# Optimization experiments

Hardware: AMD Instinct MI355X
Metric: run time of the kernel (lower is better)

The kernel has to match this reference:

```python
import jax, jax.numpy as jnp
import numpy as np

B, N, D, F_IN, E, RATIO, C, HEADS, KERNELS = 128, 512, 128, 128, 524288, 128, 10, 4, 3
ALPHA = 0.5


def setup_inputs() -> dict:
    key = jax.random.key(0)
    ks = jax.random.split(key, 20)

    def w(k, shape, fan):
        return (jax.random.normal(k, shape, jnp.float32) / np.float32(np.sqrt(fan)))

    gid = jnp.arange(E, dtype=jnp.int32) // (E // B)
    src = gid * N + jax.random.randint(ks[0], (E,), 0, N, dtype=jnp.int32)
    dst = gid * N + jax.random.randint(ks[1], (E,), 0, N, dtype=jnp.int32)
    edge_index = jnp.stack([src, dst]).astype(jnp.int32)
    return {
        'x': jax.random.normal(ks[2], (B * N, F_IN), jnp.float32),
        'edge_index': edge_index,
        'enc_w': w(ks[3], (F_IN, D), F_IN), 'enc_b': jnp.zeros((D,), jnp.float32),
        'gconv_w': w(ks[4], (3, KERNELS, D, D), D), 'gconv_b': jnp.zeros((3, KERNELS, D), jnp.float32),
        'wg1_w': w(ks[5], (D,), D), 'wg1_b': jnp.zeros((1,), jnp.float32),
        'wg2_w': w(ks[6], (D,), D), 'wg2_b': jnp.zeros((1,), jnp.float32),
        'pg1_w': w(ks[7], (D,), D), 'pg1_b': jnp.zeros((1,), jnp.float32),
        'pg2_w': w(ks[8], (D,), D), 'pg2_b': jnp.zeros((1,), jnp.float32),
        'q_w': w(ks[9], (D, D), D), 'q_b': jnp.zeros((D,), jnp.float32),
        'k_w': w(ks[10], (D, D), D), 'k_b': jnp.zeros((D,), jnp.float32),
        'v_w': w(ks[11], (D, D), D), 'v_b': jnp.zeros((D,), jnp.float32),
        'o_w': w(ks[12], (D, D), D), 'o_b': jnp.zeros((D,), jnp.float32),
        'ro_w': w(ks[13], (RATIO,), RATIO), 'ro_b': jnp.zeros((1,), jnp.float32),
        'c1_w': w(ks[14], (D, D), D), 'c1_b': jnp.zeros((D,), jnp.float32),
        'c2_w': w(ks[15], (D, C), D), 'c2_b': jnp.zeros((C,), jnp.float32),
    }


def _make_gcn(edge_index, n):
    # PyG GCNConv: add self-loops, symmetric normalization D^-1/2 (A+I) D^-1/2
    src, dst = edge_index[0], edge_index[1]
    deg = jax.ops.segment_sum(jnp.ones(src.shape[0], jnp.float32), dst, num_segments=n) + 1.0
    dinv = jax.lax.rsqrt(deg)
    norm = dinv[src] * dinv[dst]          # [E]
    self_norm = dinv * dinv               # self-loop coefficient

    def gcn(x, W, b):
        h = x @ W                                                  # [n, out]
        out = jax.ops.segment_sum(h[src] * norm[:, None], dst, num_segments=n)
        return out + h * self_norm[:, None] + b
    return gcn


def _forward(x, edge_index, enc_w, enc_b, gconv_w, gconv_b,
             wg1_w, wg1_b, wg2_w, wg2_b, pg1_w, pg1_b, pg2_w, pg2_b,
             q_w, q_b, k_w, k_b, v_w, v_b, o_w, o_b, ro_w, ro_b,
             c1_w, c1_b, c2_w, c2_b):
    n = x.shape[0]
    gcn = _make_gcn(edge_index, n)
    h = x @ enc_w + enc_b                   # node encoder (dropout: eval mode)

    def mkgc(hin, Ws, bs):                  # sum of relu(GCNConv) over kernels
        out = jax.nn.relu(gcn(hin, Ws[0], bs[0]))
        for kk in range(1, Ws.shape[0]):
            out = out + jax.nn.relu(gcn(hin, Ws[kk], bs[kk]))
        return out

    x1 = mkgc(h, gconv_w[0], gconv_b[0])
    x2 = mkgc(x1, gconv_w[1], gconv_b[1])
    x3 = mkgc(x2, gconv_w[2], gconv_b[2])

    def gla_score(xi, w1, b1, w2, b2):      # GLAPool(flag=1): global + local score
        s1 = xi @ w1[:, None] + b1          # [n,1]
        s2 = gcn(xi, w2[:, None], b2)       # [n,1]
        return ALPHA * s1 + (1.0 - ALPHA) * s2

    wts = jnp.concatenate([gla_score(xi, wg1_w, wg1_b, wg2_w, wg2_b)
                           for xi in (x1, x2, x3)], axis=-1)        # [n,3]
    wts = jax.nn.softmax(wts, axis=-1)
    xf = wts[:, 0:1] * x1 + wts[:, 1:2] * x2 + wts[:, 2:3] * x3

    # GLAPool top-k pooling (uniform graph sizes -> dense [B,N])
    score = gla_score(xf, pg1_w, pg1_b, pg2_w, pg2_b)[:, 0].reshape(B, N)
    vals, idx = jax.lax.top_k(score, RATIO)                          # [B,RATIO]
    xd = xf.reshape(B, N, D)
    xp = jnp.take_along_axis(xd, idx[:, :, None], axis=1) * jnp.tanh(vals)[:, :, None]

    # MAB: Q from pooled nodes, K/V = GCNConv over full graph
    dh = D // HEADS
    Qh = (xp @ q_w + q_b).reshape(B, RATIO, HEADS, dh)
    K = gcn(xf, k_w, k_b).reshape(B, N, HEADS, dh)
    V = gcn(xf, v_w, v_b).reshape(B, N, HEADS, dh)
    att = jnp.einsum('bqhd,bkhd->bhqk', Qh, K) / jnp.sqrt(jnp.float32(D))
    A = jax.nn.softmax(att, axis=-1)
    O = Qh + jnp.einsum('bhqk,bkhd->bqhd', A, V)
    O = O.reshape(B, RATIO, D)
    O = O + jax.nn.relu(O @ o_w + o_b)

    # Conv1d(ratio, 1, 1) readout == learned weighted sum over pooled slots
    xg = jnp.einsum('r,brd->bd', ro_w, O) + ro_b                     # [B,D]

    hc = jax.nn.relu(xg @ c1_w + c1_b)
    logp = jax.nn.log_softmax(hc @ c2_w + c2_b, axis=-1)
    return logp, xg


def reference(x, edge_index, enc_w, enc_b, gconv_w, gconv_b,
              wg1_w, wg1_b, wg2_w, wg2_b, pg1_w, pg1_b, pg2_w, pg2_b,
              q_w, q_b, k_w, k_b, v_w, v_b, o_w, o_b, ro_w, ro_b,
              c1_w, c1_b, c2_w, c2_b):
    return _forward(x, edge_index, enc_w, enc_b, gconv_w, gconv_b,
                    wg1_w, wg1_b, wg2_w, wg2_b, pg1_w, pg1_b, pg2_w, pg2_b,
                    q_w, q_b, k_w, k_b, v_w, v_b, o_w, o_b, ro_w, ro_b,
                    c1_w, c1_b, c2_w, c2_b)
```

## Files before the change

kernel.cpp:

```cpp
#include <hip/hip_runtime.h>
#include <math.h>

#define N_NODES 65536
#define NE      524288
#define DD      128
#define BGRAPH  128
#define NPG     512
#define RATIO_K 128
#define NHEAD   4
#define DHEAD   32

typedef short bf16x8 __attribute__((ext_vector_type(8)));
typedef float f32x4 __attribute__((ext_vector_type(4)));

union U8 { unsigned short u[8]; bf16x8 v; };

__device__ __forceinline__ unsigned short f2b(float f) {
  unsigned u = __float_as_uint(f);
  unsigned r = u + 0x7fffu + ((u >> 16) & 1u);
  return (unsigned short)(r >> 16);
}
__device__ __forceinline__ float b2f(unsigned short h) {
  return __uint_as_float(((unsigned)h) << 16);
}
__device__ __forceinline__ void split3(float v, unsigned short& h, unsigned short& m, unsigned short& l) {
  h = f2b(v);
  float vm = v - b2f(h);
  m = f2b(vm);
  l = f2b(vm - b2f(m));
}


__global__ void count_kernel(const int* __restrict__ dst, int* __restrict__ cnt) {
  int e = blockIdx.x * 256 + threadIdx.x;
  if (e < NE) atomicAdd(&cnt[dst[e]], 1);
}

__global__ void dinv_kernel(const int* __restrict__ cnt, float* __restrict__ dinv) {
  int i = blockIdx.x * 256 + threadIdx.x;
  if (i < N_NODES) dinv[i] = rsqrtf((float)cnt[i] + 1.0f);
}

__global__ __launch_bounds__(512) void scan_kernel2(const int* __restrict__ cnt, int* __restrict__ rp) {
  __shared__ int part[512];
  int g = blockIdx.x, t = threadIdx.x;
  int v = cnt[g * 512 + t];
  part[t] = v;
  __syncthreads();
  for (int off = 1; off < 512; off <<= 1) {
    int u = (t >= off) ? part[t - off] : 0;
    __syncthreads();
    part[t] += u;
    __syncthreads();
  }
  rp[g * 512 + t] = g * 4096 + part[t] - v;
  if (g == BGRAPH - 1 && t == 511) rp[N_NODES] = NE;
}

__global__ void scatter_kernel(const int* __restrict__ edge, const int* __restrict__ rp,
                               int* __restrict__ fill, const float* __restrict__ dinv,
                               int* __restrict__ col, float* __restrict__ wgt) {
  int e = blockIdx.x * 256 + threadIdx.x;
  if (e >= NE) return;
  int s = edge[e];
  int d = edge[NE + e];
  int p = rp[d] + atomicAdd(&fill[d], 1);
  col[p] = s;
  wgt[p] = dinv[s] * dinv[d];
}

struct WPtrs { const float* p[14]; };

__global__ void wprep_all(WPtrs wp, unsigned short* __restrict__ dstBase) {
  int mat = blockIdx.y;
  int idx = blockIdx.x * 256 + threadIdx.x;
  const float* __restrict__ W = wp.p[mat];
  unsigned short* __restrict__ dst = dstBase + (size_t)mat * 49152;
  int k = idx >> 7, n = idx & 127;
  float v = W[k * 128 + n];
  unsigned short h, m, l;
  split3(v, h, m, l);
  dst[n * 128 + k] = h;
  dst[16384 + n * 128 + k] = m;
  dst[32768 + n * 128 + k] = l;
}

#define WROW 40

template<int NW, bool RELU, bool RES, bool DUAL>
__global__ __launch_bounds__(256, 2) void mfma_gemm8(
    const float* __restrict__ A,
    const unsigned short* __restrict__ Wt,
    const float* __restrict__ bias, const float* __restrict__ bias2,
    const float* __restrict__ res,
    float* __restrict__ out, float* __restrict__ out2) {
  __shared__ unsigned short Wlds[NW * 3 * 64 * WROW];
  int tid = threadIdx.x;
  int wave = tid >> 6, lane = tid & 63;
  int c16 = lane & 15, kg = lane >> 4;
  int wrow = (wave >> 1) * 32;
  int wcol = (wave & 1) * 32;
  size_t row0 = (size_t)blockIdx.y * 64 + wrow;
  int n0 = blockIdx.x * 64;

  f32x4 acc[NW][2][2];
  #pragma unroll
  for (int m = 0; m < NW; ++m)
    #pragma unroll
    for (int mi = 0; mi < 2; ++mi)
      #pragma unroll
      for (int ni = 0; ni < 2; ++ni) acc[m][mi][ni] = (f32x4){0.f, 0.f, 0.f, 0.f};

  for (int ks = 0; ks < 4; ++ks) {
    if (ks) __syncthreads();
    #pragma unroll
    for (int i = 0; i < NW * 3; ++i) {
      int c = tid + i * 256;
      int u4 = c & 3;
      int n = (c >> 2) & 63;
      int mp = c >> 8;
      *(uint4*)&Wlds[(mp * 64 + n) * WROW + u4 * 8] =
          *(const uint4*)&Wt[(size_t)mp * 16384 + (n0 + n) * 128 + ks * 32 + u4 * 8];
    }
    __syncthreads();

    bf16x8 a[2][3];
    #pragma unroll
    for (int mi = 0; mi < 2; ++mi) {
      const float* ap = A + (row0 + mi * 16 + c16) * 128 + ks * 32 + kg * 8;
      float4 f0 = *(const float4*)ap;
      float4 f1 = *(const float4*)(ap + 4);
      float f[8] = {f0.x, f0.y, f0.z, f0.w, f1.x, f1.y, f1.z, f1.w};
      U8 hh, mm, ll;
      #pragma unroll
      for (int j = 0; j < 8; ++j) split3(f[j], hh.u[j], mm.u[j], ll.u[j]);
      a[mi][0] = hh.v; a[mi][1] = mm.v; a[mi][2] = ll.v;
    }

    #pragma unroll
    for (int mat = 0; mat < NW; ++mat) {
      #pragma unroll
      for (int ni = 0; ni < 2; ++ni) {
        int nrow = (wcol >> 4) + ni;
        int off = ((mat * 3) * 64 + nrow * 16 + c16) * WROW + kg * 8;
        bf16x8 bh = *(const bf16x8*)&Wlds[off];
        bf16x8 bm = *(const bf16x8*)&Wlds[off + 64 * WROW];
        bf16x8 bl = *(const bf16x8*)&Wlds[off + 128 * WROW];
        #pragma unroll
        for (int mi = 0; mi < 2; ++mi) {
          acc[mat][mi][ni] = __builtin_amdgcn_mfma_f32_16x16x32_bf16(a[mi][0], bh, acc[mat][mi][ni], 0, 0, 0);
          acc[mat][mi][ni] = __builtin_amdgcn_mfma_f32_16x16x32_bf16(a[mi][0], bm, acc[mat][mi][ni], 0, 0, 0);
          acc[mat][mi][ni] = __builtin_amdgcn_mfma_f32_16x16x32_bf16(a[mi][1], bh, acc[mat][mi][ni], 0, 0, 0);
          acc[mat][mi][ni] = __builtin_amdgcn_mfma_f32_16x16x32_bf16(a[mi][0], bl, acc[mat][mi][ni], 0, 0, 0);
          acc[mat][mi][ni] = __builtin_amdgcn_mfma_f32_16x16x32_bf16(a[mi][2], bh, acc[mat][mi][ni], 0, 0, 0);
          acc[mat][mi][ni] = __builtin_amdgcn_mfma_f32_16x16x32_bf16(a[mi][1], bm, acc[mat][mi][ni], 0, 0, 0);
        }
      }
    }
  }

  #pragma unroll
  for (int mi = 0; mi < 2; ++mi)
    #pragma unroll
    for (int ni = 0; ni < 2; ++ni) {
      int colg = n0 + wcol + ni * 16 + c16;
      #pragma unroll
      for (int r = 0; r < 4; ++r) {
        size_t o = (row0 + mi * 16 + kg * 4 + r) * 128 + colg;
        if (DUAL) {
          out[o]  = acc[0][mi][ni][r] + bias[colg];
          out2[o] = acc[NW - 1][mi][ni][r] + bias2[colg];
        } else if (NW == 3) {
          float g = fmaxf(acc[0][mi][ni][r] + bias[colg], 0.f)
                  + fmaxf(acc[1][mi][ni][r] + bias[128 + colg], 0.f)
                  + fmaxf(acc[2][mi][ni][r] + bias[256 + colg], 0.f);
          out[o] = g;
        } else {
          float g = acc[0][mi][ni][r] + bias[colg];
          if (RELU) g = fmaxf(g, 0.f);
          if (RES) g += res[o];
          out[o] = g;
        }
      }
    }
}

__global__ __launch_bounds__(256) void gemm_k128(
    const float* __restrict__ A, const float* __restrict__ W,
    const float* __restrict__ bias, const float* __restrict__ res,
    float* __restrict__ out, int M, int do_relu) {
  __shared__ float As[8][64];
  __shared__ float Ws[8][128];
  int tid = threadIdx.x;
  int tx = tid & 15;
  int ty = tid >> 4;
  int row0 = blockIdx.x * 64;
  if (row0 >= M) return;
  const float* Ab = A + (size_t)row0 * DD;

  float acc[4][8];
  #pragma unroll
  for (int i = 0; i < 4; ++i)
    #pragma unroll
    for (int j = 0; j < 8; ++j) acc[i][j] = 0.f;

  for (int k0 = 0; k0 < 128; k0 += 8) {
    {
      int e = tid * 2;
      int r = e >> 3, kk = e & 7;
      float2 av = *(const float2*)&Ab[r * DD + k0 + kk];
      As[kk][r] = av.x;
      As[kk + 1][r] = av.y;
    }
    {
      int kk = tid >> 5, c = (tid & 31) * 4;
      float4 wv = *(const float4*)&W[(k0 + kk) * DD + c];
      *(float4*)&Ws[kk][c] = wv;
    }
    __syncthreads();
    #pragma unroll
    for (int kk = 0; kk < 8; ++kk) {
      float4 a4 = *(const float4*)&As[kk][ty * 4];
      float4 b0 = *(const float4*)&Ws[kk][tx * 8];
      float4 b1 = *(const float4*)&Ws[kk][tx * 8 + 4];
      float av[4] = {a4.x, a4.y, a4.z, a4.w};
      float bv[8] = {b0.x, b0.y, b0.z, b0.w, b1.x, b1.y, b1.z, b1.w};
      #pragma unroll
      for (int i = 0; i < 4; ++i)
        #pragma unroll
        for (int j = 0; j < 8; ++j) acc[i][j] += av[i] * bv[j];
    }
    __syncthreads();
  }
  #pragma unroll
  for (int i = 0; i < 4; ++i) {
    int r = row0 + ty * 4 + i;
    size_t base = (size_t)r * DD + tx * 8;
    #pragma unroll
    for (int j = 0; j < 8; ++j) {
      float g = acc[i][j];
      if (bias) g += bias[tx * 8 + j];
      if (do_relu) g = fmaxf(g, 0.f);
      if (res) g += res[base + j];
      out[base + j] = g;
    }
  }
}

__global__ __launch_bounds__(256) void agg4_kernel(
    const float* __restrict__ H, const int* __restrict__ rp, const int* __restrict__ col,
    const float* __restrict__ wgt, const float* __restrict__ dinv,
    float* __restrict__ out) {
  int g = blockIdx.x * 256 + threadIdx.x;
  int node = g >> 5;
  int l = g & 31;
  const float4* H4 = (const float4*)H;
  float dv = dinv[node];
  float4 acc = H4[(size_t)node * 32 + l];
  float sn = dv * dv;
  acc.x *= sn; acc.y *= sn; acc.z *= sn; acc.w *= sn;
  int beg = rp[node], end = rp[node + 1];
  for (int j = beg; j < end; ++j) {
    float w = wgt[j];
    int c = col[j];
    float4 hv = H4[(size_t)c * 32 + l];
    acc.x += w * hv.x; acc.y += w * hv.y; acc.z += w * hv.z; acc.w += w * hv.w;
  }
  ((float4*)out)[(size_t)node * 32 + l] = acc;
}

__global__ __launch_bounds__(256) void dot2_kernel(
    const float* __restrict__ X, const float* __restrict__ w1, const float* __restrict__ w2,
    float* __restrict__ t1, float* __restrict__ t2) {
  int node = (blockIdx.x * 256 + threadIdx.x) >> 6;
  int lane = threadIdx.x & 63;
  if (node >= N_NODES) return;
  const float* xr = X + (size_t)node * DD;
  float a = xr[lane], b = xr[lane + 64];
  float s1 = a * w1[lane] + b * w1[lane + 64];
  float s2 = a * w2[lane] + b * w2[lane + 64];
  #pragma unroll
  for (int off = 32; off > 0; off >>= 1) {
    s1 += __shfl_down(s1, off);
    s2 += __shfl_down(s2, off);
  }
  if (lane == 0) { t1[node] = s1; t2[node] = s2; }
}

__global__ void score_kernel(const float* __restrict__ t1, const float* __restrict__ t2,
                             const int* __restrict__ rp, const int* __restrict__ col,
                             const float* __restrict__ wgt, const float* __restrict__ dinv,
                             const float* __restrict__ b1p, const float* __restrict__ b2p,
                             float* __restrict__ out) {
  int i = blockIdx.x * 256 + threadIdx.x;
  if (i >= N_NODES) return;
  float dv = dinv[i];
  float a2 = dv * dv * t2[i] + b2p[0];
  int beg = rp[i], end = rp[i + 1];
  for (int j = beg; j < end; ++j) a2 += wgt[j] * t2[col[j]];
  out[i] = 0.5f * (t1[i] + b1p[0]) + 0.5f * a2;
}

__global__ void xf_kernel(const float* __restrict__ x1, const float* __restrict__ x2,
                          const float* __restrict__ x3, const float* __restrict__ sc,
                          float* __restrict__ xf) {
  size_t idx = (size_t)blockIdx.x * 256 + threadIdx.x;
  int i = (int)(idx >> 5);
  float s0 = sc[i], s1 = sc[N_NODES + i], s2 = sc[2 * N_NODES + i];
  float mx = fmaxf(s0, fmaxf(s1, s2));
  float e0 = __expf(s0 - mx), e1 = __expf(s1 - mx), e2 = __expf(s2 - mx);
  float inv = 1.f / (e0 + e1 + e2);
  e0 *= inv; e1 *= inv; e2 *= inv;
  float4 a = ((const float4*)x1)[idx];
  float4 b = ((const float4*)x2)[idx];
  float4 c = ((const float4*)x3)[idx];
  float4 o;
  o.x = e0 * a.x + e1 * b.x + e2 * c.x;
  o.y = e0 * a.y + e1 * b.y + e2 * c.y;
  o.z = e0 * a.z + e1 * b.z + e2 * c.z;
  o.w = e0 * a.w + e1 * b.w + e2 * c.w;
  ((float4*)xf)[idx] = o;
}

__global__ __launch_bounds__(512) void topk_kernel(const float* __restrict__ score,
                                                   int* __restrict__ idxO, float* __restrict__ valO) {
  int b = blockIdx.x;
  int t = threadIdx.x;
  __shared__ float s[512];
  float v = score[b * NPG + t];
  s[t] = v;
  __syncthreads();
  int rank = 0;
  for (int j = 0; j < 512; ++j) {
    float u = s[j];
    rank += (u > v) || (u == v && j < t);
  }
  if (rank < RATIO_K) { idxO[b * RATIO_K + rank] = t; valO[b * RATIO_K + rank] = v; }
}

__global__ void xp_kernel(const float* __restrict__ xf, const int* __restrict__ idx,
                          const float* __restrict__ vals, float* __restrict__ xp) {
  size_t e = (size_t)blockIdx.x * 256 + threadIdx.x;
  int b = (int)(e >> 14);
  int r = (int)((e >> 7) & 127);
  int f = (int)(e & 127);
  float tv = tanhf(vals[b * RATIO_K + r]);
  int node = idx[b * RATIO_K + r];
  xp[e] = xf[((size_t)b * NPG + node) * DD + f] * tv;
}

__global__ __launch_bounds__(256) void attn_mfma_kernel(
    const float* __restrict__ Q, const float* __restrict__ K,
    const float* __restrict__ V, float* __restrict__ O) {
  int bb = blockIdx.x >> 2, h = blockIdx.x & 3;
  int tid = threadIdx.x;
  int wave = tid >> 6, lane = tid & 63;
  int c16 = lane & 15, kg = lane >> 4;
  int qbase = wave * 32;
  const float cscale = 0.088388347648318447f;

  __shared__ float Vs[64][34];
  __shared__ unsigned char PwB[4][32 * 144];

  bf16x8 Qh[2], Ql[2];
  #pragma unroll
  for (int qt = 0; qt < 2; ++qt) {
    const float* qp = Q + ((size_t)bb * 128 + qbase + qt * 16 + c16) * 128 + h * 32 + kg * 8;
    float4 f0 = *(const float4*)qp;
    float4 f1 = *(const float4*)(qp + 4);
    float f[8] = {f0.x, f0.y, f0.z, f0.w, f1.x, f1.y, f1.z, f1.w};
    U8 hh, ll;
    #pragma unroll
    for (int j = 0; j < 8; ++j) { hh.u[j] = f2b(f[j]); ll.u[j] = f2b(f[j] - b2f(hh.u[j])); }
    Qh[qt] = hh.v; Ql[qt] = ll.v;
  }

  float m2[2] = {-3.0e38f, -3.0e38f};
  float l2[2] = {0.f, 0.f};
  f32x4 od[2][2];
  #pragma unroll
  for (int dt = 0; dt < 2; ++dt)
    #pragma unroll
    for (int qt = 0; qt < 2; ++qt) od[dt][qt] = (f32x4){0.f, 0.f, 0.f, 0.f};

  for (int kc = 0; kc < NPG; kc += 64) {
    if (kc) __syncthreads();
    {
      int j = tid >> 2, grp = tid & 3;
      const float* vp = V + ((size_t)bb * NPG + kc + j) * 128 + h * 32 + grp * 8;
      float4 v0 = *(const float4*)vp;
      float4 v1 = *(const float4*)(vp + 4);
      float* d = &Vs[j][grp * 8];
      *(float2*)&d[0] = make_float2(v0.x, v0.y);
      *(float2*)&d[2] = make_float2(v0.z, v0.w);
      *(float2*)&d[4] = make_float2(v1.x, v1.y);
      *(float2*)&d[6] = make_float2(v1.z, v1.w);
    }
    __syncthreads();

    f32x4 sac[2][4];
    #pragma unroll
    for (int qt = 0; qt < 2; ++qt)
      #pragma unroll
      for (int kt = 0; kt < 4; ++kt) sac[qt][kt] = (f32x4){0.f, 0.f, 0.f, 0.f};

    #pragma unroll
    for (int kt = 0; kt < 4; ++kt) {
      const float* kp = K + ((size_t)bb * NPG + kc + kt * 16 + c16) * 128 + h * 32 + kg * 8;
      float4 f0 = *(const float4*)kp;
      float4 f1 = *(const float4*)(kp + 4);
      float f[8] = {f0.x, f0.y, f0.z, f0.w, f1.x, f1.y, f1.z, f1.w};
      U8 hh, ll;
      #pragma unroll
      for (int j = 0; j < 8; ++j) { hh.u[j] = f2b(f[j]); ll.u[j] = f2b(f[j] - b2f(hh.u[j])); }
      #pragma unroll
      for (int qt = 0; qt < 2; ++qt) {
        sac[qt][kt] = __builtin_amdgcn_mfma_f32_16x16x32_bf16(hh.v, Qh[qt], sac[qt][kt], 0, 0, 0);
        sac[qt][kt] = __builtin_amdgcn_mfma_f32_16x16x32_bf16(hh.v, Ql[qt], sac[qt][kt], 0, 0, 0);
        sac[qt][kt] = __builtin_amdgcn_mfma_f32_16x16x32_bf16(ll.v, Qh[qt], sac[qt][kt], 0, 0, 0);
      }
    }

    float pj[2][16];
    float scl2[2];
    #pragma unroll
    for (int qt = 0; qt < 2; ++qt) {
      float mc = -3.0e38f;
      #pragma unroll
      for (int kt = 0; kt < 4; ++kt)
        #pragma unroll
        for (int r = 0; r < 4; ++r) {
          float v = sac[qt][kt][r] * cscale;
          pj[qt][kt * 4 + r] = v;
          mc = fmaxf(mc, v);
        }
      mc = fmaxf(mc, __shfl_xor(mc, 16));
      mc = fmaxf(mc, __shfl_xor(mc, 32));
      float mnew = fmaxf(m2[qt], mc);
      float scl = __expf(m2[qt] - mnew);
      float ls = 0.f;
      #pragma unroll
      for (int i = 0; i < 16; ++i) {
        float e = __expf(pj[qt][i] - mnew);
        pj[qt][i] = e;
        ls += e;
      }
      ls += __shfl_xor(ls, 16);
      ls += __shfl_xor(ls, 32);
      l2[qt] = l2[qt] * scl + ls;
      m2[qt] = mnew;
      scl2[qt] = scl;
    }
    #pragma unroll
    for (int dt = 0; dt < 2; ++dt)
      #pragma unroll
      for (int qt = 0; qt < 2; ++qt) {
        #pragma unroll
        for (int r = 0; r < 4; ++r) od[dt][qt][r] *= scl2[qt];
      }

    #pragma unroll
    for (int qt = 0; qt < 2; ++qt) {
      int q32 = qt * 16 + c16;
      unsigned char* pb = &PwB[wave][q32 * 144];
      unsigned sw = (unsigned)((q32 & 7) << 4);
      #pragma unroll
      for (int kt = 0; kt < 4; ++kt)
        #pragma unroll
        for (int rp = 0; rp < 2; ++rp) {
          unsigned pk = (unsigned)f2b(pj[qt][kt * 4 + 2 * rp]) |
                        ((unsigned)f2b(pj[qt][kt * 4 + 2 * rp + 1]) << 16);
          *(unsigned*)&pb[((unsigned)(kt * 32 + kg * 8 + 4 * rp)) ^ sw] = pk;
        }
    }

    #pragma unroll
    for (int kw = 0; kw < 2; ++kw) {
      bf16x8 Pb[2];
      #pragma unroll
      for (int qt = 0; qt < 2; ++qt) {
        int q32 = qt * 16 + c16;
        Pb[qt] = *(const bf16x8*)&PwB[wave][q32 * 144 +
                   (((unsigned)(kw * 64 + kg * 16)) ^ ((unsigned)((q32 & 7) << 4)))];
      }
      #pragma unroll
      for (int dt = 0; dt < 2; ++dt) {
        U8 vh, vl;
        #pragma unroll
        for (int j = 0; j < 8; ++j) {
          float v = Vs[kw * 32 + kg * 8 + j][dt * 16 + c16];
          vh.u[j] = f2b(v);
          vl.u[j] = f2b(v - b2f(vh.u[j]));
        }
        #pragma unroll
        for (int qt = 0; qt < 2; ++qt) {
          od[dt][qt] = __builtin_amdgcn_mfma_f32_16x16x32_bf16(vh.v, Pb[qt], od[dt][qt], 0, 0, 0);
          od[dt][qt] = __builtin_amdgcn_mfma_f32_16x16x32_bf16(vl.v, Pb[qt], od[dt][qt], 0, 0, 0);
        }
      }
    }
  }

  #pragma unroll
  for (int qt = 0; qt < 2; ++qt) {
    float inv = 1.f / l2[qt];
    size_t row = (size_t)bb * 128 + qbase + qt * 16 + c16;
    #pragma unroll
    for (int dt = 0; dt < 2; ++dt)
      #pragma unroll
      for (int r = 0; r < 4; ++r) {
        int colg = h * 32 + dt * 16 + kg * 4 + r;
        O[row * 128 + colg] = Q[row * 128 + colg] + od[dt][qt][r] * inv;
      }
  }
}

__global__ void readout_kernel(const float* __restrict__ O2, const float* __restrict__ ro_w,
                               const float* __restrict__ ro_b, float* __restrict__ xg) {
  int idx = blockIdx.x * 256 + threadIdx.x;
  int b = idx >> 7, d = idx & 127;
  float s = ro_b[0];
  for (int r = 0; r < RATIO_K; ++r) s += ro_w[r] * O2[((size_t)b * RATIO_K + r) * DD + d];
  xg[idx] = s;
}

__global__ __launch_bounds__(64) void head_kernel(const float* __restrict__ hc,
                                                  const float* __restrict__ c2w,
                                                  const float* __restrict__ c2b,
                                                  float* __restrict__ out) {
  int b = blockIdx.x, t = threadIdx.x;
  __shared__ float z[10];
  __shared__ float lse_s;
  if (t < 10) {
    float s = c2b[t];
    for (int k = 0; k < 128; ++k) s += hc[b * 128 + k] * c2w[k * 10 + t];
    z[t] = s;
  }
  __syncthreads();
  if (t == 0) {
    float mx = z[0];
    for (int c = 1; c < 10; ++c) mx = fmaxf(mx, z[c]);
    float sum = 0.f;
    for (int c = 0; c < 10; ++c) sum += expf(z[c] - mx);
    lse_s = mx + logf(sum);
  }
  __syncthreads();
  if (t < 10) out[b * 10 + t] = z[t] - lse_s;
}

extern "C" void kernel_launch(void* const* d_in, const int* in_sizes, int n_in,
                              void* d_out, int out_size, void* d_ws, size_t ws_size,
                              hipStream_t stream) {
  const float* x       = (const float*)d_in[0];
  const int*   edge    = (const int*)d_in[1];
  const float* enc_w   = (const float*)d_in[2];
  const float* enc_b   = (const float*)d_in[3];
  const float* gconv_w = (const float*)d_in[4];
  const float* gconv_b = (const float*)d_in[5];
  const float* wg1_w   = (const float*)d_in[6];
  const float* wg1_b   = (const float*)d_in[7];
  const float* wg2_w   = (const float*)d_in[8];
  const float* wg2_b   = (const float*)d_in[9];
  const float* pg1_w   = (const float*)d_in[10];
  const float* pg1_b   = (const float*)d_in[11];
  const float* pg2_w   = (const float*)d_in[12];
  const float* pg2_b   = (const float*)d_in[13];
  const float* q_w     = (const float*)d_in[14];
  const float* q_b     = (const float*)d_in[15];
  const float* k_w     = (const float*)d_in[16];
  const float* k_b     = (const float*)d_in[17];
  const float* v_w     = (const float*)d_in[18];
  const float* v_b     = (const float*)d_in[19];
  const float* o_w     = (const float*)d_in[20];
  const float* o_b     = (const float*)d_in[21];
  const float* ro_w    = (const float*)d_in[22];
  const float* ro_b    = (const float*)d_in[23];
  const float* c1_w    = (const float*)d_in[24];
  const float* c1_b    = (const float*)d_in[25];
  const float* c2_w    = (const float*)d_in[26];
  const float* c2_b    = (const float*)d_in[27];

  float* outp = (float*)d_out;

  const size_t S = (size_t)N_NODES * DD;
  float* ws    = (float*)d_ws;
  float* slot0 = ws;
  float* slot1 = ws + S;
  float* slot2 = ws + 2 * S;
  float* slot3 = ws + 3 * S;
  float* smallf = ws + 4 * S;
  int*   cnt  = (int*)smallf;
  int*   fill = cnt + N_NODES;
  int*   rp   = fill + N_NODES;
  int*   col  = rp + N_NODES + 8;
  float* wgt  = (float*)(col + NE);
  float* dinv = wgt + NE;
  float* sc   = dinv + N_NODES;
  float* t1   = sc + 3 * N_NODES;
  float* t2   = t1 + N_NODES;
  float* score = t2 + N_NODES;
  int*   tidx = (int*)(score + N_NODES);
  float* tval = (float*)(tidx + BGRAPH * RATIO_K);
  float* hcbuf = tval + BGRAPH * RATIO_K;
  unsigned short* wsW = (unsigned short*)(hcbuf + BGRAPH * DD);
  float* aggbuf = (float*)(wsW + 14 * 49152);

  const size_t SP = (size_t)BGRAPH * RATIO_K * DD;
  float* xp = slot3;
  float* Qm = slot3 + SP;
  float* Om = slot3 + 2 * SP;
  float* O2 = slot3 + 3 * SP;

  hipMemsetAsync(cnt, 0, N_NODES * sizeof(int), stream);
  hipMemsetAsync(fill, 0, N_NODES * sizeof(int), stream);
  count_kernel<<<NE / 256, 256, 0, stream>>>(edge + NE, cnt);
  dinv_kernel<<<N_NODES / 256, 256, 0, stream>>>(cnt, dinv);
  scan_kernel2<<<BGRAPH, 512, 0, stream>>>(cnt, rp);
  scatter_kernel<<<NE / 256, 256, 0, stream>>>(edge, rp, fill, dinv, col, wgt);

  WPtrs wp;
  wp.p[0] = enc_w;
  for (int i = 0; i < 9; ++i) wp.p[1 + i] = gconv_w + (size_t)i * DD * DD;
  wp.p[10] = k_w; wp.p[11] = v_w; wp.p[12] = q_w; wp.p[13] = o_w;
  wprep_all<<<dim3(64, 14), 256, 0, stream>>>(wp, wsW);

  mfma_gemm8<1, false, false, false><<<dim3(2, 1024), 256, 0, stream>>>(
      x, wsW, enc_b, nullptr, nullptr, slot0, nullptr);

  float* lin[4] = {slot0, slot1, slot2, slot3};
  const int AGG_GRID = (N_NODES * 32) / 256;
  for (int l = 0; l < 3; ++l) {
    const float* hin = lin[l];
    float* hout = lin[l + 1];
    agg4_kernel<<<AGG_GRID, 256, 0, stream>>>(hin, rp, col, wgt, dinv, aggbuf);
    mfma_gemm8<3, true, false, false><<<dim3(2, 1024), 256, 0, stream>>>(
        aggbuf, wsW + (size_t)(1 + l * 3) * 49152, gconv_b + (size_t)l * 3 * DD,
        nullptr, nullptr, hout, nullptr);
    dot2_kernel<<<N_NODES / 4, 256, 0, stream>>>(hout, wg1_w, wg2_w, t1, t2);
    score_kernel<<<N_NODES / 256, 256, 0, stream>>>(t1, t2, rp, col, wgt, dinv, wg1_b, wg2_b, sc + (size_t)l * N_NODES);
  }

  float* xf = slot0;
  xf_kernel<<<(N_NODES * 32) / 256, 256, 0, stream>>>(slot1, slot2, slot3, sc, xf);

  dot2_kernel<<<N_NODES / 4, 256, 0, stream>>>(xf, pg1_w, pg2_w, t1, t2);
  score_kernel<<<N_NODES / 256, 256, 0, stream>>>(t1, t2, rp, col, wgt, dinv, pg1_b, pg2_b, score);
  topk_kernel<<<BGRAPH, 512, 0, stream>>>(score, tidx, tval);
  xp_kernel<<<(BGRAPH * RATIO_K * DD) / 256, 256, 0, stream>>>(xf, tidx, tval, xp);

  mfma_gemm8<1, false, false, false><<<dim3(2, 256), 256, 0, stream>>>(
      xp, wsW + 12 * 49152UL, q_b, nullptr, nullptr, Qm, nullptr);

  agg4_kernel<<<AGG_GRID, 256, 0, stream>>>(xf, rp, col, wgt, dinv, aggbuf);
  mfma_gemm8<2, false, false, true><<<dim3(2, 1024), 256, 0, stream>>>(
      aggbuf, wsW + 10 * 49152UL, k_b, v_b, nullptr, slot1, slot2);

  attn_mfma_kernel<<<BGRAPH * NHEAD, 256, 0, stream>>>(Qm, slot1, slot2, Om);

  mfma_gemm8<1, true, true, false><<<dim3(2, 256), 256, 0, stream>>>(
      Om, wsW + 13 * 49152UL, o_b, nullptr, Om, O2, nullptr);

  float* xg = outp + BGRAPH * 10;
  readout_kernel<<<(BGRAPH * DD) / 256, 256, 0, stream>>>(O2, ro_w, ro_b, xg);

  gemm_k128<<<BGRAPH / 64, 256, 0, stream>>>(xg, c1_w, c1_b, nullptr, hcbuf, BGRAPH, 1);
  head_kernel<<<BGRAPH, 64, 0, stream>>>(hcbuf, c2_w, c2_b, outp);
}
```

Measured before the change: 677.2 us.

## Double-buffer weight LDS tiles with register prefetch in split-bf16 MFMA GEMM

Restructures the GEMM weight staging into per-(k-slice, matrix) stages. Each stage's weight tile is double-buffered in LDS and the next-next tile is prefetched into registers, so global loads overlap with the MFMA work. The LDS row pitch drops from 40 to 36 and the footprint shrinks to two single-matrix buffers, which allows launch bounds of 3 blocks per CU for more occupancy. The trade-off is more barriers (one per stage rather than one per k-slice) and higher register pressure under the tighter launch bound.

```diff
diff --git a/kernel.cpp b/kernel.cpp
--- a/kernel.cpp
+++ b/kernel.cpp
@@ -85,16 +85,17 @@
   dst[32768 + n * 128 + k] = l;
 }
 
-#define WROW 40
+#define WROW9 36
 
 template<int NW, bool RELU, bool RES, bool DUAL>
-__global__ __launch_bounds__(256, 2) void mfma_gemm8(
+__global__ __launch_bounds__(256, 3) void mfma_gemm9(
     const float* __restrict__ A,
     const unsigned short* __restrict__ Wt,
     const float* __restrict__ bias, const float* __restrict__ bias2,
     const float* __restrict__ res,
     float* __restrict__ out, float* __restrict__ out2) {
-  __shared__ unsigned short Wlds[NW * 3 * 64 * WROW];
+  __shared__ unsigned short Wlds[2][3 * 64 * WROW9];
+  const int NS = NW * 4;
   int tid = threadIdx.x;
   int wave = tid >> 6, lane = tid & 63;
   int c16 = lane & 15, kg = lane >> 4;
@@ -102,6 +103,7 @@
   int wcol = (wave & 1) * 32;
   size_t row0 = (size_t)blockIdx.y * 64 + wrow;
   int n0 = blockIdx.x * 64;
+  int u4 = tid & 3, nst = tid >> 2;
 
   f32x4 acc[NW][2][2];
   #pragma unroll
@@ -111,52 +113,74 @@
       #pragma unroll
       for (int ni = 0; ni < 2; ++ni) acc[m][mi][ni] = (f32x4){0.f, 0.f, 0.f, 0.f};
 
-  for (int ks = 0; ks < 4; ++ks) {
-    if (ks) __syncthreads();
-    #pragma unroll
-    for (int i = 0; i < NW * 3; ++i) {
-      int c = tid + i * 256;
-      int u4 = c & 3;
-      int n = (c >> 2) & 63;
-      int mp = c >> 8;
-      *(uint4*)&Wlds[(mp * 64 + n) * WROW + u4 * 8] =
-          *(const uint4*)&Wt[(size_t)mp * 16384 + (n0 + n) * 128 + ks * 32 + u4 * 8];
+  uint4 pr[3];
+  #pragma unroll
+  for (int p = 0; p < 3; ++p)
+    pr[p] = *(const uint4*)&Wt[(size_t)p * 16384 + (n0 + nst) * 128 + u4 * 8];
+  #pragma unroll
+  for (int p = 0; p < 3; ++p)
+    *(uint4*)&Wlds[0][(p * 64 + nst) * WROW9 + u4 * 8] = pr[p];
+  if (NS > 1) {
+    const int ks1 = 1 / NW, mat1 = 1 % NW;
+    #pragma unroll
+    for (int p = 0; p < 3; ++p)
+      pr[p] = *(const uint4*)&Wt[(size_t)mat1 * 49152 + (size_t)p * 16384 +
+                                 (n0 + nst) * 128 + ks1 * 32 + u4 * 8];
+  }
+  __syncthreads();
+
+  bf16x8 a[2][3];
+  #pragma unroll
+  for (int s = 0; s < NS; ++s) {
+    const int cur = s & 1;
+    const int ks = s / NW, mat = s % NW;
+
+    if (s + 1 < NS) {
+      #pragma unroll
+      for (int p = 0; p < 3; ++p)
+        *(uint4*)&Wlds[cur ^ 1][(p * 64 + nst) * WROW9 + u4 * 8] = pr[p];
+    }
+
+    if (mat == 0) {
+      #pragma unroll
+      for (int mi = 0; mi < 2; ++mi) {
+        const float* ap = A + (row0 + mi * 16 + c16) * 128 + ks * 32 + kg * 8;
+        float4 f0 = *(const float4*)ap;
+        float4 f1 = *(const float4*)(ap + 4);
+        float f[8] = {f0.x, f0.y, f0.z, f0.w, f1.x, f1.y, f1.z, f1.w};
+        U8 hh, mm, ll;
+        #pragma unroll
+        for (int j = 0; j < 8; ++j) split3(f[j], hh.u[j], mm.u[j], ll.u[j]);
+        a[mi][0] = hh.v; a[mi][1] = mm.v; a[mi][2] = ll.v;
+      }
+    }
+
+    if (s + 2 < NS) {
+      const int ks2 = (s + 2) / NW, mat2 = (s + 2) % NW;
+      #pragma unroll
+      for (int p = 0; p < 3; ++p)
+        pr[p] = *(const uint4*)&Wt[(size_t)mat2 * 49152 + (size_t)p * 16384 +
+                                   (n0 + nst) * 128 + ks2 * 32 + u4 * 8];
+    }
+
+    #pragma unroll
+    for (int ni = 0; ni < 2; ++ni) {
+      int nrow = (wcol >> 4) + ni;
+      int off = (nrow * 16 + c16) * WROW9 + kg * 8;
+      bf16x8 bh = *(const bf16x8*)&Wlds[cur][off];
+      bf16x8 bm = *(const bf16x8*)&Wlds[cur][off + 64 * WROW9];
+      bf16x8 bl = *(const bf16x8*)&Wlds[cur][off + 128 * WROW9];
+      #pragma unroll
+      for (int mi = 0; mi < 2; ++mi) {
+        acc[mat][mi][ni] = __builtin_amdgcn_mfma_f32_16x16x32_bf16(a[mi][0], bh, acc[mat][mi][ni], 0, 0, 0);
+        acc[mat][mi][ni] = __builtin_amdgcn_mfma_f32_16x16x32_bf16(a[mi][0], bm, acc[mat][mi][ni], 0, 0, 0);
+        acc[mat][mi][ni] = __builtin_amdgcn_mfma_f32_16x16x32_bf16(a[mi][1], bh, acc[mat][mi][ni], 0, 0, 0);
+        acc[mat][mi][ni] = __builtin_amdgcn_mfma_f32_16x16x32_bf16(a[mi][0], bl, acc[mat][mi][ni], 0, 0, 0);
+        acc[mat][mi][ni] = __builtin_amdgcn_mfma_f32_16x16x32_bf16(a[mi][2], bh, acc[mat][mi][ni], 0, 0, 0);
+        acc[mat][mi][ni] = __builtin_amdgcn_mfma_f32_16x16x32_bf16(a[mi][1], bm, acc[mat][mi][ni], 0, 0, 0);
+      }
     }
     __syncthreads();
-
-    bf16x8 a[2][3];
-    #pragma unroll
-    for (int mi = 0; mi < 2; ++mi) {
-      const float* ap = A + (row0 + mi * 16 + c16) * 128 + ks * 32 + kg * 8;
-      float4 f0 = *(const float4*)ap;
-      float4 f1 = *(const float4*)(ap + 4);
-      float f[8] = {f0.x, f0.y, f0.z, f0.w, f1.x, f1.y, f1.z, f1.w};
-      U8 hh, mm, ll;
-      #pragma unroll
-      for (int j = 0; j < 8; ++j) split3(f[j], hh.u[j], mm.u[j], ll.u[j]);
-      a[mi][0] = hh.v; a[mi][1] = mm.v; a[mi][2] = ll.v;
-    }
-
-    #pragma unroll
-    for (int mat = 0; mat < NW; ++mat) {
-      #pragma unroll
-      for (int ni = 0; ni < 2; ++ni) {
-        int nrow = (wcol >> 4) + ni;
-        int off = ((mat * 3) * 64 + nrow * 16 + c16) * WROW + kg * 8;
-        bf16x8 bh = *(const bf16x8*)&Wlds[off];
-        bf16x8 bm = *(const bf16x8*)&Wlds[off + 64 * WROW];
-        bf16x8 bl = *(const bf16x8*)&Wlds[off + 128 * WROW];
-        #pragma unroll
-        for (int mi = 0; mi < 2; ++mi) {
-          acc[mat][mi][ni] = __builtin_amdgcn_mfma_f32_16x16x32_bf16(a[mi][0], bh, acc[mat][mi][ni], 0, 0, 0);
-          acc[mat][mi][ni] = __builtin_amdgcn_mfma_f32_16x16x32_bf16(a[mi][0], bm, acc[mat][mi][ni], 0, 0, 0);
-          acc[mat][mi][ni] = __builtin_amdgcn_mfma_f32_16x16x32_bf16(a[mi][1], bh, acc[mat][mi][ni], 0, 0, 0);
-          acc[mat][mi][ni] = __builtin_amdgcn_mfma_f32_16x16x32_bf16(a[mi][0], bl, acc[mat][mi][ni], 0, 0, 0);
-          acc[mat][mi][ni] = __builtin_amdgcn_mfma_f32_16x16x32_bf16(a[mi][2], bh, acc[mat][mi][ni], 0, 0, 0);
-          acc[mat][mi][ni] = __builtin_amdgcn_mfma_f32_16x16x32_bf16(a[mi][1], bm, acc[mat][mi][ni], 0, 0, 0);
-        }
-      }
-    }
   }
 
   #pragma unroll
@@ -624,7 +648,7 @@
   wp.p[10] = k_w; wp.p[11] = v_w; wp.p[12] = q_w; wp.p[13] = o_w;
   wprep_all<<<dim3(64, 14), 256, 0, stream>>>(wp, wsW);
 
-  mfma_gemm8<1, false, false, false><<<dim3(2, 1024), 256, 0, stream>>>(
+  mfma_gemm9<1, false, false, false><<<dim3(2, 1024), 256, 0, stream>>>(
       x, wsW, enc_b, nullptr, nullptr, slot0, nullptr);
 
   float* lin[4] = {slot0, slot1, slot2, slot3};
@@ -633,7 +657,7 @@
     const float* hin = lin[l];
     float* hout = lin[l + 1];
     agg4_kernel<<<AGG_GRID, 256, 0, stream>>>(hin, rp, col, wgt, dinv, aggbuf);
-    mfma_gemm8<3, true, false, false><<<dim3(2, 1024), 256, 0, stream>>>(
+    mfma_gemm9<3, true, false, false><<<dim3(2, 1024), 256, 0, stream>>>(
         aggbuf, wsW + (size_t)(1 + l * 3) * 49152, gconv_b + (size_t)l * 3 * DD,
         nullptr, nullptr, hout, nullptr);
     dot2_kernel<<<N_NODES / 4, 256, 0, stream>>>(hout, wg1_w, wg2_w, t1, t2);
@@ -648,16 +672,16 @@
   topk_kernel<<<BGRAPH, 512, 0, stream>>>(score, tidx, tval);
   xp_kernel<<<(BGRAPH * RATIO_K * DD) / 256, 256, 0, stream>>>(xf, tidx, tval, xp);
 
-  mfma_gemm8<1, false, false, false><<<dim3(2, 256), 256, 0, stream>>>(
+  mfma_gemm9<1, false, false, false><<<dim3(2, 256), 256, 0, stream>>>(
       xp, wsW + 12 * 49152UL, q_b, nullptr, nullptr, Qm, nullptr);
 
   agg4_kernel<<<AGG_GRID, 256, 0, stream>>>(xf, rp, col, wgt, dinv, aggbuf);
-  mfma_gemm8<2, false, false, true><<<dim3(2, 1024), 256, 0, stream>>>(
+  mfma_gemm9<2, false, false, true><<<dim3(2, 1024), 256, 0, stream>>>(
       aggbuf, wsW + 10 * 49152UL, k_b, v_b, nullptr, slot1, slot2);
 
   attn_mfma_kernel<<<BGRAPH * NHEAD, 256, 0, stream>>>(Qm, slot1, slot2, Om);
 
-  mfma_gemm8<1, true, true, false><<<dim3(2, 256), 256, 0, stream>>>(
+  mfma_gemm9<1, true, true, false><<<dim3(2, 256), 256, 0, stream>>>(
       Om, wsW + 13 * 49152UL, o_b, nullptr, Om, O2, nullptr);
 
   float* xg = outp + BGRAPH * 10;
```

Result: slower. 833.1 us (+23.0%).
